# Optimization experiments

Measured on AMD Instinct MI355X. Metric: run time of the kernel, lower is better.

The kernel has to match this reference:

```python
import jax, jax.numpy as jnp
import numpy as np

INV_PI = 0.31830988618
PI_over_2 = 1.57079632679
PI_over_4 = 0.78539816339
N_MODES, DIM, COND_C = 8, 2, 64
LAYERS = [COND_C, 128, 512, 128, 32, N_MODES * DIM * 2 + N_MODES + 1]
N = 262144


def setup_inputs() -> dict:
    key = jax.random.key(0)
    ks = jax.random.split(key, 2 + 2 * (len(LAYERS) - 1))
    inp = {}
    inp["cond_vec"] = jax.random.normal(ks[0], (N, COND_C), jnp.float32)
    # uniforms in (0,1), bounded away from 0/1 so log/div are finite
    inp["randseed"] = jax.random.uniform(ks[1], (N, 2), jnp.float32, 1e-4, 1.0 - 1e-4)
    for i in range(len(LAYERS) - 1):
        inp[f"W{i}"] = jax.random.normal(ks[2 + 2 * i], (LAYERS[i], LAYERS[i + 1]), jnp.float32) * 0.01
        inp[f"b{i}"] = jnp.zeros((LAYERS[i + 1],), jnp.float32)
    return inp


def _mlp(x, Ws, bs):
    for i, (W, b) in enumerate(zip(Ws, bs)):
        x = x @ W + b
        if i < len(Ws) - 1:
            x = jax.nn.relu(x)
    return x


def _forward(cond_vec, randseed, Ws, bs):
    nm, d = N_MODES, DIM
    h = _mlp(cond_vec, Ws, bs)  # [N, nm*d*2 + nm + 1]
    loc = h[:, : nm * d].reshape(-1, nm, d)
    log_scale = h[:, nm * d : 2 * nm * d].reshape(-1, nm, d)
    w = jnp.abs(h[:, 2 * nm * d :])
    w = w / jnp.sum(w, axis=1, keepdims=True)  # [N, nm+1]
    wL = w[:, -1]

    r0, r1 = randseed[:, 0], randseed[:, 1]
    lambert_mask = r0 < wL
    gauss_mask = ~lambert_mask
    # in-place rescale of randseed column 0 in the torch code
    u0 = jnp.where(lambert_mask, r0 / wL, (r0 - wL) / (1.0 - wL))

    # --- gauss branch (Box-Muller) ---
    U1 = jnp.where(gauss_mask, u0, 0.5)  # masked positions: safe dummy
    U1 = jnp.maximum(U1, 1e-12)
    R = jnp.sqrt(-2.0 * jnp.log(U1))
    th = 2.0 * jnp.pi * r1
    eps_ = jnp.stack([R * jnp.cos(th), R * jnp.sin(th)], axis=-1)  # [N, 2]
    scale_sample = jnp.sum(jnp.exp(log_scale), axis=1)  # [N, 2]
    loc_sample = jnp.sum(loc, axis=1)  # [N, 2]
    z_gauss = eps_ * scale_sample + loc_sample

    # --- lambert branch (concentric disk map) ---
    wo0 = u0 * 2.0 - 1.0
    wo1 = r1 * 2.0 - 1.0
    nonzero = ~((wo0 == 0) & (wo1 == 0))
    cond1 = (jnp.abs(wo0) > jnp.abs(wo1)) & nonzero
    cond2 = (~cond1) & nonzero
    safe0 = jnp.where(wo0 == 0, 1.0, wo0)
    safe1 = jnp.where(wo1 == 0, 1.0, wo1)
    phi = jnp.where(cond1, PI_over_4 * wo1 / safe0, PI_over_2 - PI_over_4 * wo0 / safe1)
    r = jnp.where(cond1, wo0, jnp.where(cond2, wo1, 0.0))
    z_lambert = jnp.stack([r * jnp.cos(phi), r * jnp.sin(phi)], axis=-1)

    z = jnp.where(lambert_mask[:, None], z_lambert, z_gauss)  # [N, 2]

    # --- mixture log prob ---
    eps = (z[:, None, :] - loc) / jnp.exp(log_scale)  # [N, nm, 2]
    log_p = (-0.5 * d * jnp.log(2.0 * jnp.pi)
             + jnp.log(w[:, :-1] + 1e-5)
             - 0.5 * jnp.sum(eps ** 2, axis=2)
             - jnp.sum(log_scale, axis=2))  # [N, nm]
    pdf = jnp.where(z[:, 0] ** 2 + z[:, 1] ** 2 > 1.0, 0.0, INV_PI)
    lambert_log_p = jnp.log(pdf + 1e-5) + jnp.log(wL)
    log_p = jnp.concatenate([log_p, lambert_log_p[:, None]], axis=-1)  # [N, nm+1]
    return z, jax.scipy.special.logsumexp(log_p, axis=1)


def reference(cond_vec, randseed, W0, b0, W1, b1, W2, b2, W3, b3, W4, b4):
    Ws = [W0, W1, W2, W3, W4]
    bs = [b0, b1, b2, b3, b4]
    return _forward(cond_vec, randseed, Ws, bs)
```

## Files before the change

### kernel.cpp

```cpp
#include <hip/hip_runtime.h>
#include <math.h>

#define NTOT 262144
#define BROWS 64
#define THREADS 512
#define PITCH 140

typedef short bf16x8 __attribute__((ext_vector_type(8)));
typedef float f32x16 __attribute__((ext_vector_type(16)));

#define O0H 0
#define O0L 8192
#define O1H 16384
#define O1L 81920
#define O2H 147456
#define O2L 212992
#define GCNT_OFF 557056
#define GLIST_OFF 557120

#define SOFTBAR() asm volatile("s_waitcnt lgkmcnt(0)\n\ts_barrier" ::: "memory")

#define WAITV(N) do{ asm volatile("s_waitcnt vmcnt(" #N ")" ::: "memory"); \
                     __builtin_amdgcn_sched_barrier(0); }while(0)

#define LOADG4(r0, r1, r2, r3, base) do{ \
    asm volatile("global_load_dwordx4 %0, %1, %2 offset:0"    : "=v"(r0) : "v"(voff), "s"(base)); \
    asm volatile("global_load_dwordx4 %0, %1, %2 offset:1024" : "=v"(r1) : "v"(voff), "s"(base)); \
    asm volatile("global_load_dwordx4 %0, %1, %2 offset:2048" : "=v"(r2) : "v"(voff), "s"(base)); \
    asm volatile("global_load_dwordx4 %0, %1, %2 offset:3072" : "=v"(r3) : "v"(voff), "s"(base)); \
}while(0)

__device__ __forceinline__ unsigned short bf16_rne(float x){
    unsigned u = __float_as_uint(x);
    return (unsigned short)((u + 0x7FFFu + ((u >> 16) & 1u)) >> 16);
}
__device__ __forceinline__ void split2(float x, unsigned short& h, unsigned short& l){
    h = bf16_rne(x);
    float xh = __uint_as_float(((unsigned)h) << 16);
    l = bf16_rne(x - xh);
}

__device__ __forceinline__ int frag_off(int n, int k, int nks){
    return ((((n >> 5) * nks + (k >> 4)) << 9) | (((k >> 3) & 1) << 8) | ((n & 31) << 3) | (k & 7));
}

__global__ void prep_weights(const float* __restrict__ W0, const float* __restrict__ W1,
                             const float* __restrict__ W2, unsigned short* __restrict__ ws){
    int i = blockIdx.x * 256 + threadIdx.x;
    float v; int oh, ol;
    if (i < 8192){
        int n = i >> 6, k = i & 63; v = W0[k*128 + n];
        int o = frag_off(n, k, 4);  oh = O0H + o; ol = O0L + o;
    } else if (i < 73728){
        int j = i - 8192; int n = j >> 7, k = j & 127; v = W1[k*512 + n];
        int o = frag_off(n, k, 8);  oh = O1H + o; ol = O1L + o;
    } else if (i < 139264){
        int j = i - 73728; int n = j >> 9, k = j & 511; v = W2[k*128 + n];
        int o = frag_off(n, k, 32); oh = O2H + o; ol = O2L + o;
    } else return;
    unsigned short h, l; split2(v, h, l);
    ws[oh] = h; ws[ol] = l;
}

__device__ __forceinline__ void epilogue_row(const float* __restrict__ h, float r0v, float r1v,
        float& z0o, float& z1o, float& lseo, float& wLo, float& u0o, bool& lamo){
    float wraw[9]; float wsum = 0.0f;
    #pragma unroll
    for (int j = 0; j < 9; ++j){ wraw[j] = fabsf(h[32 + j]); wsum += wraw[j]; }
    float wL = wraw[8] / wsum;
    const bool lambert = r0v < wL;
    float u0 = lambert ? (r0v / wL) : ((r0v - wL) / (1.0f - wL));
    float U1 = lambert ? 0.5f : u0;
    U1 = fmaxf(U1, 1e-12f);
    float R  = sqrtf(-2.0f * logf(U1));
    float th = 6.28318530717958647692f * r1v;
    float ce = cosf(th), se = sinf(th);
    float es0[8], es1[8];
    float ssum0 = 0.0f, ssum1 = 0.0f, lsum0 = 0.0f, lsum1 = 0.0f;
    #pragma unroll
    for (int m = 0; m < 8; ++m){
        es0[m] = expf(h[16 + 2*m]); es1[m] = expf(h[16 + 2*m + 1]);
        ssum0 += es0[m]; ssum1 += es1[m];
        lsum0 += h[2*m]; lsum1 += h[2*m + 1];
    }
    float zg0 = (R * ce) * ssum0 + lsum0;
    float zg1 = (R * se) * ssum1 + lsum1;
    float wo0 = u0 * 2.0f - 1.0f;
    float wo1 = r1v * 2.0f - 1.0f;
    bool nonzero = !((wo0 == 0.0f) && (wo1 == 0.0f));
    bool c1 = (fabsf(wo0) > fabsf(wo1)) && nonzero;
    bool c2 = (!c1) && nonzero;
    float sa0 = (wo0 == 0.0f) ? 1.0f : wo0;
    float sa1 = (wo1 == 0.0f) ? 1.0f : wo1;
    float phi = c1 ? (0.78539816339f * wo1 / sa0)
                   : (1.57079632679f - 0.78539816339f * wo0 / sa1);
    float rr = c1 ? wo0 : (c2 ? wo1 : 0.0f);
    float zl0 = rr * cosf(phi);
    float zl1 = rr * sinf(phi);
    float z0 = lambert ? zl0 : zg0;
    float z1 = lambert ? zl1 : zg1;
    float lp[9];
    #pragma unroll
    for (int m = 0; m < 8; ++m){
        float e0 = (z0 - h[2*m])     / es0[m];
        float e1 = (z1 - h[2*m + 1]) / es1[m];
        float wm = wraw[m] / wsum;
        lp[m] = (-1.83787706640934548356f + logf(wm + 1e-5f))
                - 0.5f * (e0*e0 + e1*e1)
                - (h[16 + 2*m] + h[16 + 2*m + 1]);
    }
    float pdf = (z0*z0 + z1*z1 > 1.0f) ? 0.0f : 0.31830988618f;
    lp[8] = logf(pdf + 1e-5f) + logf(wL);
    float mx = lp[0];
    #pragma unroll
    for (int j = 1; j < 9; ++j) mx = fmaxf(mx, lp[j]);
    float s = 0.0f;
    #pragma unroll
    for (int j = 0; j < 9; ++j) s += expf(lp[j] - mx);
    z0o = z0; z1o = z1; lseo = mx + logf(s); wLo = wL; u0o = u0; lamo = lambert;
}

__device__ __forceinline__ bool flag_row(float r0v, float z0, float z1, float wL, float u0, bool lam){
    return (fabsf(r0v - wL) < 5e-3f)
        || (wL < 3e-3f) || (wL > 0.5f)
        || (fabsf(z0*z0 + z1*z1 - 1.0f) < (lam ? 0.02f : 0.2f))
        || (!lam && u0 < 3e-3f);
}

__device__ __forceinline__ f32x16 bias_init(const float* __restrict__ b, int mt, int lane, int nmax){
    f32x16 c;
    const int hq = ((lane >> 5) << 2);
    #pragma unroll
    for (int r = 0; r < 16; ++r){
        int n = mt + (r & 3) + ((r >> 2) << 3) + hq;
        c[r] = (n < nmax) ? b[n] : 0.0f;
    }
    return c;
}

__device__ __forceinline__ void write_tile(unsigned short* __restrict__ ah, unsigned short* __restrict__ al,
        int brow, int m0, int lane, const f32x16 acc, bool relu){
    const int hq = ((lane >> 5) << 2);
    #pragma unroll
    for (int q = 0; q < 4; ++q){
        ushort4 vh, vl;
        #pragma unroll
        for (int r = 0; r < 4; ++r){
            float x = acc[q*4 + r];
            if (relu) x = fmaxf(x, 0.0f);
            unsigned short hh, ll; split2(x, hh, ll);
            (&vh.x)[r] = hh; (&vl.x)[r] = ll;
        }
        const int off = brow*PITCH + m0 + q*8 + hq;
        *(ushort4*)(ah + off) = vh;
        *(ushort4*)(al + off) = vl;
    }
}

__device__ __forceinline__ void write_tile_f32t(float* __restrict__ dst,
        int brow, int m0, int lane, const f32x16 acc){
    const int hq = ((lane >> 5) << 2);
    #pragma unroll
    for (int q = 0; q < 4; ++q){
        #pragma unroll
        for (int r = 0; r < 4; ++r){
            int n = m0 + q*8 + hq + r;
            dst[n*64 + brow] = fmaxf(acc[q*4 + r], 0.0f);
        }
    }
}

__device__ __forceinline__ void mfma_half(const bf16x8* wh, const bf16x8* wl,
        const unsigned short* __restrict__ acth, const unsigned short* __restrict__ actl,
        int ks0, int brow, int lane, f32x16& acc){
    const int kl = ((lane >> 5) << 3);
    #pragma unroll
    for (int i = 0; i < 4; ++i){
        const int k0 = (ks0 + i)*16 + kl;
        bf16x8 ah = *(const bf16x8*)(acth + brow*PITCH + k0);
        bf16x8 al = *(const bf16x8*)(actl + brow*PITCH + k0);
        acc = __builtin_amdgcn_mfma_f32_32x32x16_bf16(wh[i], ah, acc, 0, 0, 0);
        acc = __builtin_amdgcn_mfma_f32_32x32x16_bf16(wh[i], al, acc, 0, 0, 0);
        acc = __builtin_amdgcn_mfma_f32_32x32x16_bf16(wl[i], ah, acc, 0, 0, 0);
    }
}

__global__ __launch_bounds__(THREADS, 4)
void gmm_mfma(const float* __restrict__ cond, const float* __restrict__ rnd,
              const unsigned short* __restrict__ ws,
              const float* __restrict__ b0, const float* __restrict__ b1,
              const float* __restrict__ b2,
              const float* __restrict__ W3, const float* __restrict__ b3,
              const float* __restrict__ W4, const float* __restrict__ b4,
              int* __restrict__ gcnt, int* __restrict__ glist,
              float* __restrict__ out)
{
    extern __shared__ unsigned char smem[];
    unsigned short* aAh = (unsigned short*)smem;
    unsigned short* aAl = aAh + 64*PITCH;
    unsigned short* aBh = aAl + 64*PITCH;
    unsigned short* aBl = aBh + 64*PITCH;
    float* h2f = (float*)smem;
    float* h3f = (float*)(smem + 35840);
    float* h4f = (float*)(smem + 44032);
    float* b1g = (float*)(smem + 71680);
    float* b2g = b1g + 512;

    const int tid  = threadIdx.x;
    const int lane = tid & 63;
    const int wv   = tid >> 6;
    const int row0 = blockIdx.x * BROWS;
    const int rg   = wv & 1;
    const int ct   = wv >> 1;
    const int brow = rg*32 + (lane & 31);
    const int m0   = ct * 32;
    const int kl   = ((lane >> 5) << 3);
    const unsigned voff = (unsigned)lane * 16;

    bf16x8 whA[4], wlA[4], whB[4], wlB[4];

    b1g[tid >= 512 ? 0 : tid] = b1[tid >= 512 ? 0 : tid];
    if (tid < 128) b2g[tid] = b2[tid];

    {
        f32x16 acc0 = bias_init(b0, m0, lane, 128);
        #pragma unroll 2
        for (int ks = 0; ks < 4; ++ks){
            const int k0 = ks*16 + kl;
            const float* cp = cond + (size_t)(row0 + brow)*64 + k0;
            float4 ca = *(const float4*)cp;
            float4 cb = *(const float4*)(cp + 4);
            float xs[8] = {ca.x, ca.y, ca.z, ca.w, cb.x, cb.y, cb.z, cb.w};
            bf16x8 ah, al;
            #pragma unroll
            for (int j = 0; j < 8; ++j){
                unsigned short hh, ll; split2(xs[j], hh, ll);
                ah[j] = (short)hh; al[j] = (short)ll;
            }
            bf16x8 wh = *(const bf16x8*)(ws + O0H + (ct*4 + ks)*512 + lane*8);
            bf16x8 wl = *(const bf16x8*)(ws + O0L + (ct*4 + ks)*512 + lane*8);
            acc0 = __builtin_amdgcn_mfma_f32_32x32x16_bf16(wh, ah, acc0, 0, 0, 0);
            acc0 = __builtin_amdgcn_mfma_f32_32x32x16_bf16(wh, al, acc0, 0, 0, 0);
            acc0 = __builtin_amdgcn_mfma_f32_32x32x16_bf16(wl, ah, acc0, 0, 0, 0);
        }
        write_tile(aAh, aAl, brow, m0, lane, acc0, true);
    }

    asm volatile("s_waitcnt vmcnt(0)" ::: "memory");
    __builtin_amdgcn_sched_barrier(0);
    {
        const unsigned short* p1h = ws + O1H + __builtin_amdgcn_readfirstlane(ct*4096);
        const unsigned short* p1l = ws + O1L + __builtin_amdgcn_readfirstlane(ct*4096);
        LOADG4(whA[0], whA[1], whA[2], whA[3], p1h);
        LOADG4(wlA[0], wlA[1], wlA[2], wlA[3], p1l);
    }
    SOFTBAR();

    f32x16 acc2 = bias_init(b2g, m0, lane, 128);
    #pragma unroll
    for (int c = 0; c < 4; ++c){
        const unsigned short* b1h = ws + O1H + __builtin_amdgcn_readfirstlane((c*4 + ct)*4096);
        const unsigned short* b1l = ws + O1L + __builtin_amdgcn_readfirstlane((c*4 + ct)*4096);
        const unsigned short* c2h = ws + O2H + __builtin_amdgcn_readfirstlane((ct*32 + c*8)*512);
        const unsigned short* c2l = ws + O2L + __builtin_amdgcn_readfirstlane((ct*32 + c*8)*512);

        LOADG4(whB[0], whB[1], whB[2], whB[3], b1h + 2048);
        LOADG4(wlB[0], wlB[1], wlB[2], wlB[3], b1l + 2048);
        WAITV(8);
        f32x16 a1 = bias_init(b1g + c*128, m0, lane, 128);
        mfma_half(whA, wlA, aAh, aAl, 0, brow, lane, a1);

        LOADG4(whA[0], whA[1], whA[2], whA[3], c2h);
        LOADG4(wlA[0], wlA[1], wlA[2], wlA[3], c2l);
        WAITV(8);
        mfma_half(whB, wlB, aAh, aAl, 4, brow, lane, a1);

        LOADG4(whB[0], whB[1], whB[2], whB[3], c2h + 2048);
        LOADG4(wlB[0], wlB[1], wlB[2], wlB[3], c2l + 2048);
        SOFTBAR();
        write_tile(aBh, aBl, brow, m0, lane, a1, true);
        SOFTBAR();
        WAITV(8);
        mfma_half(whA, wlA, aBh, aBl, 0, brow, lane, acc2);

        if (c < 3){
            const unsigned short* n1h = ws + O1H + __builtin_amdgcn_readfirstlane(((c+1)*4 + ct)*4096);
            const unsigned short* n1l = ws + O1L + __builtin_amdgcn_readfirstlane(((c+1)*4 + ct)*4096);
            LOADG4(whA[0], whA[1], whA[2], whA[3], n1h);
            LOADG4(wlA[0], wlA[1], wlA[2], wlA[3], n1l);
            WAITV(8);
        } else {
            WAITV(0);
        }
        mfma_half(whB, wlB, aBh, aBl, 4, brow, lane, acc2);
    }
    write_tile_f32t(h2f, brow, m0, lane, acc2);
    SOFTBAR();

    {
        const int row = tid & 63;
        const int nb  = tid >> 6;
        float acc[4];
        #pragma unroll
        for (int c = 0; c < 4; ++c) acc[c] = b3[nb*4 + c];
        #pragma unroll 8
        for (int k = 0; k < 128; ++k){
            float a = h2f[k*64 + row];
            const float* wr = W3 + k*32 + nb*4;
            #pragma unroll
            for (int c = 0; c < 4; ++c) acc[c] = fmaf(a, wr[c], acc[c]);
        }
        SOFTBAR();
        #pragma unroll
        for (int c = 0; c < 4; ++c) h3f[(nb*4 + c)*64 + row] = fmaxf(acc[c], 0.0f);
    }
    SOFTBAR();

    {
        const int row = tid & 63;
        const int nb  = tid >> 6;
        float acc[6];
        #pragma unroll
        for (int c = 0; c < 6; ++c){ int n = nb*6 + c; acc[c] = (n < 41) ? b4[n] : 0.0f; }
        #pragma unroll 8
        for (int k = 0; k < 32; ++k){
            float a = h3f[k*64 + row];
            const float* wr = W4 + k*41;
            #pragma unroll
            for (int c = 0; c < 6; ++c){ int n = nb*6 + c; if (n < 41) acc[c] = fmaf(a, wr[n], acc[c]); }
        }
        #pragma unroll
        for (int c = 0; c < 6; ++c){ int n = nb*6 + c; if (n < 41) h4f[n*64 + row] = acc[c]; }
    }
    SOFTBAR();

    if (tid < 64){
        const int row  = tid;
        const int grow = row0 + row;
        float h[41];
        #pragma unroll
        for (int j = 0; j < 41; ++j) h[j] = h4f[j*64 + row];
        float2 rv = *(const float2*)(rnd + 2*(size_t)grow);
        float z0, z1, lse, wL, u0; bool lam;
        epilogue_row(h, rv.x, rv.y, z0, z1, lse, wL, u0, lam);
        ((float2*)out)[grow] = make_float2(z0, z1);
        out[(size_t)2*NTOT + grow] = lse;
        if (flag_row(rv.x, z0, z1, wL, u0, lam)){
            int idx = atomicAdd(gcnt, 1); glist[idx] = grow;
        }
    }
}

__global__ __launch_bounds__(512, 2)
void gmm_fix(const float* __restrict__ cond, const float* __restrict__ rnd,
             const float* __restrict__ W0, const float* __restrict__ b0,
             const float* __restrict__ W1, const float* __restrict__ b1,
             const float* __restrict__ W2, const float* __restrict__ b2,
             const float* __restrict__ W3, const float* __restrict__ b3,
             const float* __restrict__ W4, const float* __restrict__ b4,
             const int* __restrict__ gcnt, const int* __restrict__ glist,
             float* __restrict__ out)
{
    __shared__ float fb[7296];
    float* c0g = fb;
    float* f0g = fb + 512;
    float* f1g = fb + 1536;
    float* f2g = fb + 5632;
    float* f3g = fb + 6656;
    float* h4g = fb + 6912;
    const int tid = threadIdx.x;
    const int nflag = *gcnt;

    for (int base = blockIdx.x * 8; base < nflag; base += gridDim.x * 8){
        const int g = min(8, nflag - base);
        {
            int i = tid >> 6, k = tid & 63;
            if (i < g) c0g[i*64 + k] = cond[(size_t)glist[base + i]*64 + k];
        }
        __syncthreads();
        if (tid < 128){
            float acc[8];
            #pragma unroll
            for (int i = 0; i < 8; ++i) acc[i] = b0[tid];
            #pragma unroll 8
            for (int k = 0; k < 64; ++k){
                float w = W0[k*128 + tid];
                #pragma unroll
                for (int i = 0; i < 8; ++i) acc[i] = fmaf(c0g[i*64 + k], w, acc[i]);
            }
            for (int i = 0; i < g; ++i) f0g[i*128 + tid] = fmaxf(acc[i], 0.0f);
        }
        __syncthreads();
        {
            float acc[8];
            #pragma unroll
            for (int i = 0; i < 8; ++i) acc[i] = b1[tid];
            #pragma unroll 8
            for (int k = 0; k < 128; ++k){
                float w = W1[k*512 + tid];
                #pragma unroll
                for (int i = 0; i < 8; ++i) acc[i] = fmaf(f0g[i*128 + k], w, acc[i]);
            }
            for (int i = 0; i < g; ++i) f1g[i*512 + tid] = fmaxf(acc[i], 0.0f);
        }
        __syncthreads();
        if (tid < 128){
            float acc[8];
            #pragma unroll
            for (int i = 0; i < 8; ++i) acc[i] = b2[tid];
            #pragma unroll 8
            for (int k = 0; k < 512; ++k){
                float w = W2[k*128 + tid];
                #pragma unroll
                for (int i = 0; i < 8; ++i) acc[i] = fmaf(f1g[i*512 + k], w, acc[i]);
            }
            for (int i = 0; i < g; ++i) f2g[i*128 + tid] = fmaxf(acc[i], 0.0f);
        }
        __syncthreads();
        if (tid < 32){
            float acc[8];
            #pragma unroll
            for (int i = 0; i < 8; ++i) acc[i] = b3[tid];
            #pragma unroll 8
            for (int k = 0; k < 128; ++k){
                float w = W3[k*32 + tid];
                #pragma unroll
                for (int i = 0; i < 8; ++i) acc[i] = fmaf(f2g[i*128 + k], w, acc[i]);
            }
            for (int i = 0; i < g; ++i) f3g[i*32 + tid] = fmaxf(acc[i], 0.0f);
        }
        __syncthreads();
        if (tid < 41){
            float acc[8];
            #pragma unroll
            for (int i = 0; i < 8; ++i) acc[i] = b4[tid];
            #pragma unroll 8
            for (int k = 0; k < 32; ++k){
                float w = W4[k*41 + tid];
                #pragma unroll
                for (int i = 0; i < 8; ++i) acc[i] = fmaf(f3g[i*32 + k], w, acc[i]);
            }
            for (int i = 0; i < g; ++i) h4g[i*48 + tid] = acc[i];
        }
        __syncthreads();
        if (tid < g){
            const int grow = glist[base + tid];
            float2 rv = *(const float2*)(rnd + 2*(size_t)grow);
            float z0, z1, lse, wL, u0; bool lam;
            epilogue_row(&h4g[tid*48], rv.x, rv.y, z0, z1, lse, wL, u0, lam);
            ((float2*)out)[grow] = make_float2(z0, z1);
            out[(size_t)2*NTOT + grow] = lse;
        }
        __syncthreads();
    }
}

extern "C" void kernel_launch(void* const* d_in, const int* in_sizes, int n_in,
                              void* d_out, int out_size, void* d_ws, size_t ws_size,
                              hipStream_t stream) {
    const float* cond = (const float*)d_in[0];
    const float* rnd  = (const float*)d_in[1];
    const float* W0 = (const float*)d_in[2];  const float* b0 = (const float*)d_in[3];
    const float* W1 = (const float*)d_in[4];  const float* b1 = (const float*)d_in[5];
    const float* W2 = (const float*)d_in[6];  const float* b2 = (const float*)d_in[7];
    const float* W3 = (const float*)d_in[8];  const float* b3 = (const float*)d_in[9];
    const float* W4 = (const float*)d_in[10]; const float* b4 = (const float*)d_in[11];
    float* out = (float*)d_out;
    unsigned short* ws = (unsigned short*)d_ws;
    int* gcnt  = (int*)((char*)d_ws + GCNT_OFF);
    int* glist = (int*)((char*)d_ws + GLIST_OFF);

    hipMemsetAsync(gcnt, 0, 4, stream);
    hipLaunchKernelGGL(prep_weights, dim3(544), dim3(256), 0, stream, W0, W1, W2, ws);

    hipLaunchKernelGGL(gmm_mfma, dim3(NTOT / BROWS), dim3(THREADS), 74240, stream,
                       cond, rnd, ws, b0, b1, b2, W3, b3, W4, b4, gcnt, glist, out);

    hipLaunchKernelGGL(gmm_fix, dim3(1024), dim3(512), 0, stream,
                       cond, rnd, W0, b0, W1, b1, W2, b2, W3, b3, W4, b4, gcnt, glist, out);
}
```

Baseline: 841.9 us.

## Halve block to four waves, each computing two row tiles per weight fragment

The block drops from 8 to 4 waves. Each wave now processes both 32-row halves of the 64-row tile, so every weight fragment loaded from global memory feeds two MFMA accumulator chains. This halves per-row weight load traffic and interleaves independent MFMAs, with s_setprio raised around the MFMA bursts. The trade-offs are higher register pressure (launch bounds lowered to 2 blocks), an unroll-1 outer loop, and a smaller LDS pitch that may change bank conflicts. The scalar tail layers also do twice the work per thread.

```diff
diff --git a/kernel.cpp b/kernel.cpp
--- a/kernel.cpp
+++ b/kernel.cpp
@@ -3,8 +3,8 @@
 
 #define NTOT 262144
 #define BROWS 64
-#define THREADS 512
-#define PITCH 140
+#define THREADS 256
+#define PITCH 132
 
 typedef short bf16x8 __attribute__((ext_vector_type(8)));
 typedef float f32x16 __attribute__((ext_vector_type(16)));
@@ -19,10 +19,8 @@
 #define GLIST_OFF 557120
 
 #define SOFTBAR() asm volatile("s_waitcnt lgkmcnt(0)\n\ts_barrier" ::: "memory")
-
 #define WAITV(N) do{ asm volatile("s_waitcnt vmcnt(" #N ")" ::: "memory"); \
                      __builtin_amdgcn_sched_barrier(0); }while(0)
-
 #define LOADG4(r0, r1, r2, r3, base) do{ \
     asm volatile("global_load_dwordx4 %0, %1, %2 offset:0"    : "=v"(r0) : "v"(voff), "s"(base)); \
     asm volatile("global_load_dwordx4 %0, %1, %2 offset:1024" : "=v"(r1) : "v"(voff), "s"(base)); \
@@ -170,22 +168,29 @@
     }
 }
 
-__device__ __forceinline__ void mfma_half(const bf16x8* wh, const bf16x8* wl,
+__device__ __forceinline__ void mfma_half2(const bf16x8* wh, const bf16x8* wl,
         const unsigned short* __restrict__ acth, const unsigned short* __restrict__ actl,
-        int ks0, int brow, int lane, f32x16& acc){
+        int ks0, int brow, int lane, f32x16& accA, f32x16& accB){
     const int kl = ((lane >> 5) << 3);
+    __builtin_amdgcn_s_setprio(1);
     #pragma unroll
     for (int i = 0; i < 4; ++i){
         const int k0 = (ks0 + i)*16 + kl;
-        bf16x8 ah = *(const bf16x8*)(acth + brow*PITCH + k0);
-        bf16x8 al = *(const bf16x8*)(actl + brow*PITCH + k0);
-        acc = __builtin_amdgcn_mfma_f32_32x32x16_bf16(wh[i], ah, acc, 0, 0, 0);
-        acc = __builtin_amdgcn_mfma_f32_32x32x16_bf16(wh[i], al, acc, 0, 0, 0);
-        acc = __builtin_amdgcn_mfma_f32_32x32x16_bf16(wl[i], ah, acc, 0, 0, 0);
-    }
-}
-
-__global__ __launch_bounds__(THREADS, 4)
+        bf16x8 a0h = *(const bf16x8*)(acth + brow*PITCH + k0);
+        bf16x8 a0l = *(const bf16x8*)(actl + brow*PITCH + k0);
+        bf16x8 a1h = *(const bf16x8*)(acth + (brow+32)*PITCH + k0);
+        bf16x8 a1l = *(const bf16x8*)(actl + (brow+32)*PITCH + k0);
+        accA = __builtin_amdgcn_mfma_f32_32x32x16_bf16(wh[i], a0h, accA, 0, 0, 0);
+        accB = __builtin_amdgcn_mfma_f32_32x32x16_bf16(wh[i], a1h, accB, 0, 0, 0);
+        accA = __builtin_amdgcn_mfma_f32_32x32x16_bf16(wh[i], a0l, accA, 0, 0, 0);
+        accB = __builtin_amdgcn_mfma_f32_32x32x16_bf16(wh[i], a1l, accB, 0, 0, 0);
+        accA = __builtin_amdgcn_mfma_f32_32x32x16_bf16(wl[i], a0h, accA, 0, 0, 0);
+        accB = __builtin_amdgcn_mfma_f32_32x32x16_bf16(wl[i], a1h, accB, 0, 0, 0);
+    }
+    __builtin_amdgcn_s_setprio(0);
+}
+
+__global__ __launch_bounds__(THREADS, 2)
 void gmm_mfma(const float* __restrict__ cond, const float* __restrict__ rnd,
               const unsigned short* __restrict__ ws,
               const float* __restrict__ b0, const float* __restrict__ b1,
@@ -201,49 +206,57 @@
     unsigned short* aBh = aAl + 64*PITCH;
     unsigned short* aBl = aBh + 64*PITCH;
     float* h2f = (float*)smem;
-    float* h3f = (float*)(smem + 35840);
-    float* h4f = (float*)(smem + 44032);
-    float* b1g = (float*)(smem + 71680);
+    float* h3f = (float*)(smem + 32768);
+    float* h4f = (float*)(smem + 40960);
+    float* b1g = (float*)(smem + 67584);
     float* b2g = b1g + 512;
 
     const int tid  = threadIdx.x;
     const int lane = tid & 63;
     const int wv   = tid >> 6;
     const int row0 = blockIdx.x * BROWS;
-    const int rg   = wv & 1;
-    const int ct   = wv >> 1;
-    const int brow = rg*32 + (lane & 31);
+    const int ct   = wv;
+    const int brow = lane & 31;
     const int m0   = ct * 32;
     const int kl   = ((lane >> 5) << 3);
     const unsigned voff = (unsigned)lane * 16;
 
     bf16x8 whA[4], wlA[4], whB[4], wlB[4];
 
-    b1g[tid >= 512 ? 0 : tid] = b1[tid >= 512 ? 0 : tid];
+    b1g[tid] = b1[tid];
+    b1g[tid + 256] = b1[tid + 256];
     if (tid < 128) b2g[tid] = b2[tid];
 
     {
-        f32x16 acc0 = bias_init(b0, m0, lane, 128);
+        f32x16 acc0a = bias_init(b0, m0, lane, 128);
+        f32x16 acc0b = acc0a;
         #pragma unroll 2
         for (int ks = 0; ks < 4; ++ks){
             const int k0 = ks*16 + kl;
-            const float* cp = cond + (size_t)(row0 + brow)*64 + k0;
-            float4 ca = *(const float4*)cp;
-            float4 cb = *(const float4*)(cp + 4);
-            float xs[8] = {ca.x, ca.y, ca.z, ca.w, cb.x, cb.y, cb.z, cb.w};
-            bf16x8 ah, al;
+            const float* cp0 = cond + (size_t)(row0 + brow)*64 + k0;
+            const float* cp1 = cond + (size_t)(row0 + brow + 32)*64 + k0;
+            float4 ca0 = *(const float4*)cp0, cb0 = *(const float4*)(cp0 + 4);
+            float4 ca1 = *(const float4*)cp1, cb1 = *(const float4*)(cp1 + 4);
+            float xs0[8] = {ca0.x, ca0.y, ca0.z, ca0.w, cb0.x, cb0.y, cb0.z, cb0.w};
+            float xs1[8] = {ca1.x, ca1.y, ca1.z, ca1.w, cb1.x, cb1.y, cb1.z, cb1.w};
+            bf16x8 a0h, a0l, a1h, a1l;
             #pragma unroll
             for (int j = 0; j < 8; ++j){
-                unsigned short hh, ll; split2(xs[j], hh, ll);
-                ah[j] = (short)hh; al[j] = (short)ll;
+                unsigned short hh, ll;
+                split2(xs0[j], hh, ll); a0h[j] = (short)hh; a0l[j] = (short)ll;
+                split2(xs1[j], hh, ll); a1h[j] = (short)hh; a1l[j] = (short)ll;
             }
             bf16x8 wh = *(const bf16x8*)(ws + O0H + (ct*4 + ks)*512 + lane*8);
             bf16x8 wl = *(const bf16x8*)(ws + O0L + (ct*4 + ks)*512 + lane*8);
-            acc0 = __builtin_amdgcn_mfma_f32_32x32x16_bf16(wh, ah, acc0, 0, 0, 0);
-            acc0 = __builtin_amdgcn_mfma_f32_32x32x16_bf16(wh, al, acc0, 0, 0, 0);
-            acc0 = __builtin_amdgcn_mfma_f32_32x32x16_bf16(wl, ah, acc0, 0, 0, 0);
-        }
-        write_tile(aAh, aAl, brow, m0, lane, acc0, true);
+            acc0a = __builtin_amdgcn_mfma_f32_32x32x16_bf16(wh, a0h, acc0a, 0, 0, 0);
+            acc0b = __builtin_amdgcn_mfma_f32_32x32x16_bf16(wh, a1h, acc0b, 0, 0, 0);
+            acc0a = __builtin_amdgcn_mfma_f32_32x32x16_bf16(wh, a0l, acc0a, 0, 0, 0);
+            acc0b = __builtin_amdgcn_mfma_f32_32x32x16_bf16(wh, a1l, acc0b, 0, 0, 0);
+            acc0a = __builtin_amdgcn_mfma_f32_32x32x16_bf16(wl, a0h, acc0a, 0, 0, 0);
+            acc0b = __builtin_amdgcn_mfma_f32_32x32x16_bf16(wl, a1h, acc0b, 0, 0, 0);
+        }
+        write_tile(aAh, aAl, brow,      m0, lane, acc0a, true);
+        write_tile(aAh, aAl, brow + 32, m0, lane, acc0b, true);
     }
 
     asm volatile("s_waitcnt vmcnt(0)" ::: "memory");
@@ -256,8 +269,9 @@
     }
     SOFTBAR();
 
-    f32x16 acc2 = bias_init(b2g, m0, lane, 128);
-    #pragma unroll
+    f32x16 acc2a = bias_init(b2g, m0, lane, 128);
+    f32x16 acc2b = acc2a;
+    #pragma unroll 1
     for (int c = 0; c < 4; ++c){
         const unsigned short* b1h = ws + O1H + __builtin_amdgcn_readfirstlane((c*4 + ct)*4096);
         const unsigned short* b1l = ws + O1L + __builtin_amdgcn_readfirstlane((c*4 + ct)*4096);
@@ -267,21 +281,23 @@
         LOADG4(whB[0], whB[1], whB[2], whB[3], b1h + 2048);
         LOADG4(wlB[0], wlB[1], wlB[2], wlB[3], b1l + 2048);
         WAITV(8);
-        f32x16 a1 = bias_init(b1g + c*128, m0, lane, 128);
-        mfma_half(whA, wlA, aAh, aAl, 0, brow, lane, a1);
+        f32x16 a1a = bias_init(b1g + c*128, m0, lane, 128);
+        f32x16 a1b = a1a;
+        mfma_half2(whA, wlA, aAh, aAl, 0, brow, lane, a1a, a1b);
 
         LOADG4(whA[0], whA[1], whA[2], whA[3], c2h);
         LOADG4(wlA[0], wlA[1], wlA[2], wlA[3], c2l);
         WAITV(8);
-        mfma_half(whB, wlB, aAh, aAl, 4, brow, lane, a1);
+        mfma_half2(whB, wlB, aAh, aAl, 4, brow, lane, a1a, a1b);
 
         LOADG4(whB[0], whB[1], whB[2], whB[3], c2h + 2048);
         LOADG4(wlB[0], wlB[1], wlB[2], wlB[3], c2l + 2048);
         SOFTBAR();
-        write_tile(aBh, aBl, brow, m0, lane, a1, true);
+        write_tile(aBh, aBl, brow,      m0, lane, a1a, true);
+        write_tile(aBh, aBl, brow + 32, m0, lane, a1b, true);
         SOFTBAR();
         WAITV(8);
-        mfma_half(whA, wlA, aBh, aBl, 0, brow, lane, acc2);
+        mfma_half2(whA, wlA, aBh, aBl, 0, brow, lane, acc2a, acc2b);
 
         if (c < 3){
             const unsigned short* n1h = ws + O1H + __builtin_amdgcn_readfirstlane(((c+1)*4 + ct)*4096);
@@ -292,45 +308,47 @@
         } else {
             WAITV(0);
         }
-        mfma_half(whB, wlB, aBh, aBl, 4, brow, lane, acc2);
-    }
-    write_tile_f32t(h2f, brow, m0, lane, acc2);
+        mfma_half2(whB, wlB, aBh, aBl, 4, brow, lane, acc2a, acc2b);
+    }
+    SOFTBAR();
+    write_tile_f32t(h2f, brow,      m0, lane, acc2a);
+    write_tile_f32t(h2f, brow + 32, m0, lane, acc2b);
     SOFTBAR();
 
     {
         const int row = tid & 63;
         const int nb  = tid >> 6;
-        float acc[4];
-        #pragma unroll
-        for (int c = 0; c < 4; ++c) acc[c] = b3[nb*4 + c];
-        #pragma unroll 8
+        float acc[8];
+        #pragma unroll
+        for (int c = 0; c < 8; ++c) acc[c] = b3[nb*8 + c];
+        #pragma unroll 4
         for (int k = 0; k < 128; ++k){
             float a = h2f[k*64 + row];
-            const float* wr = W3 + k*32 + nb*4;
-            #pragma unroll
-            for (int c = 0; c < 4; ++c) acc[c] = fmaf(a, wr[c], acc[c]);
+            const float* wr = W3 + k*32 + nb*8;
+            #pragma unroll
+            for (int c = 0; c < 8; ++c) acc[c] = fmaf(a, wr[c], acc[c]);
         }
         SOFTBAR();
         #pragma unroll
-        for (int c = 0; c < 4; ++c) h3f[(nb*4 + c)*64 + row] = fmaxf(acc[c], 0.0f);
+        for (int c = 0; c < 8; ++c) h3f[(nb*8 + c)*64 + row] = fmaxf(acc[c], 0.0f);
     }
     SOFTBAR();
 
     {
         const int row = tid & 63;
         const int nb  = tid >> 6;
-        float acc[6];
-        #pragma unroll
-        for (int c = 0; c < 6; ++c){ int n = nb*6 + c; acc[c] = (n < 41) ? b4[n] : 0.0f; }
-        #pragma unroll 8
+        float acc[11];
+        #pragma unroll
+        for (int c = 0; c < 11; ++c){ int n = nb*11 + c; acc[c] = (n < 41) ? b4[n] : 0.0f; }
+        #pragma unroll 4
         for (int k = 0; k < 32; ++k){
             float a = h3f[k*64 + row];
             const float* wr = W4 + k*41;
             #pragma unroll
-            for (int c = 0; c < 6; ++c){ int n = nb*6 + c; if (n < 41) acc[c] = fmaf(a, wr[n], acc[c]); }
-        }
-        #pragma unroll
-        for (int c = 0; c < 6; ++c){ int n = nb*6 + c; if (n < 41) h4f[n*64 + row] = acc[c]; }
+            for (int c = 0; c < 11; ++c){ int n = nb*11 + c; if (n < 41) acc[c] = fmaf(a, wr[n], acc[c]); }
+        }
+        #pragma unroll
+        for (int c = 0; c < 11; ++c){ int n = nb*11 + c; if (n < 41) h4f[n*64 + row] = acc[c]; }
     }
     SOFTBAR();
 
@@ -470,10 +488,10 @@
     int* gcnt  = (int*)((char*)d_ws + GCNT_OFF);
     int* glist = (int*)((char*)d_ws + GLIST_OFF);
 
-    hipMemsetAsync(gcnt, 0, 4, stream);
+    (void)hipMemsetAsync(gcnt, 0, 4, stream);
     hipLaunchKernelGGL(prep_weights, dim3(544), dim3(256), 0, stream, W0, W1, W2, ws);
 
-    hipLaunchKernelGGL(gmm_mfma, dim3(NTOT / BROWS), dim3(THREADS), 74240, stream,
+    hipLaunchKernelGGL(gmm_mfma, dim3(NTOT / BROWS), dim3(THREADS), 70144, stream,
                        cond, rnd, ws, b0, b1, b2, W3, b3, W4, b4, gcnt, glist, out);
 
     hipLaunchKernelGGL(gmm_fix, dim3(1024), dim3(512), 0, stream,
```

New measurement: 987.7 us. 1.17x slower.
